# Kernel tuning notes

Hardware: AMD Instinct MI355X
Metric: run time of the kernel (lower is better)

The kernel has to match this reference:

```python
import jax, jax.numpy as jnp
import numpy as np

D = 512          # input_dim == hidden size of MinLSTM layers
OUT = 1          # output_dim of fc_out
B, T = 8, 4096
LN_EPS = 1e-5


def _linear_params(key, d_in, d_out):
    kw, kb = jax.random.split(key)
    lim = 1.0 / np.sqrt(d_in)
    W = jax.random.uniform(kw, (d_out, d_in), minval=-lim, maxval=lim, dtype=jnp.float32)
    b = jax.random.uniform(kb, (d_out,), minval=-lim, maxval=lim, dtype=jnp.float32)
    return W, b


def setup_inputs() -> dict:
    key = jax.random.key(0)
    ks = jax.random.split(key, 8)
    x = jax.random.normal(ks[0], (B, T, D), dtype=jnp.float32)
    Wf0, bf0 = _linear_params(ks[1], D, D)
    Wi0, bi0 = _linear_params(ks[2], D, D)
    Wh0, bh0 = _linear_params(ks[3], D, D)
    Wf1, bf1 = _linear_params(ks[4], D, D)
    Wi1, bi1 = _linear_params(ks[5], D, D)
    Wh1, bh1 = _linear_params(ks[6], D, D)
    W_out, b_out = _linear_params(ks[7], D, OUT)
    ln_g = jnp.ones((D,), dtype=jnp.float32)
    ln_b = jnp.zeros((D,), dtype=jnp.float32)
    return {
        'x': x,
        'Wf0': Wf0, 'bf0': bf0, 'Wi0': Wi0, 'bi0': bi0, 'Wh0': Wh0, 'bh0': bh0,
        'Wf1': Wf1, 'bf1': bf1, 'Wi1': Wi1, 'bi1': bi1, 'Wh1': Wh1, 'bh1': bh1,
        'ln_g': ln_g, 'ln_b': ln_b, 'W_out': W_out, 'b_out': b_out,
    }


def _minlstm(x, Wf, bf, Wi, bi, Wh, bh):
    # minLSTM (parallel form, h0 = 0):
    #   f = sigma(W_f x), i = sigma(W_i x), h~ = W_h x
    #   f' = f/(f+i), i' = i/(f+i)
    #   h_t = f'_t * h_{t-1} + i'_t * h~_t   (linear recurrence -> associative scan)
    f = jax.nn.sigmoid(jnp.einsum('btd,ed->bte', x, Wf) + bf)
    i = jax.nn.sigmoid(jnp.einsum('btd,ed->bte', x, Wi) + bi)
    h_tilde = jnp.einsum('btd,ed->bte', x, Wh) + bh
    denom = f + i
    a = f / denom                      # decay coefficient f'
    u = (i / denom) * h_tilde          # input contribution i' * h~

    def combine(c1, c2):
        a1, u1 = c1
        a2, u2 = c2
        return a1 * a2, a2 * u1 + u2

    _, h = jax.lax.associative_scan(combine, (a, u), axis=1)
    return h  # [B, T, D]


def reference(x, Wf0, bf0, Wi0, bi0, Wh0, bh0,
              Wf1, bf1, Wi1, bi1, Wh1, bh1,
              ln_g, ln_b, W_out, b_out):
    h = _minlstm(x, Wf0, bf0, Wi0, bi0, Wh0, bh0)
    h = _minlstm(h, Wf1, bf1, Wi1, bi1, Wh1, bh1)
    h = jnp.where(jnp.isnan(h), x, h)      # NaN fallback to input
    h = x + h                               # residual
    # LayerNorm over last dim
    mu = jnp.mean(h, axis=-1, keepdims=True)
    var = jnp.mean(jnp.square(h - mu), axis=-1, keepdims=True)
    hn = (h - mu) * jax.lax.rsqrt(var + LN_EPS) * ln_g + ln_b
    # output projection [B, T, OUT]
    return jnp.einsum('btd,od->bto', hn, W_out) + b_out
```

## Files before the change

### kernel.cpp

```cpp
#include <hip/hip_runtime.h>
#include <hip/hip_bf16.h>
#include <stdint.h>


#define MROWS 32768
#define DDIM  512
#define TLEN  4096
#define BSZ   8
#define NCHUNK 64
#define CLEN   64

typedef __attribute__((ext_vector_type(8))) __bf16 bf16x8;
typedef __attribute__((ext_vector_type(16))) float f32x16;

static __device__ __forceinline__ unsigned short f2bf(float f) {
    unsigned int u = __float_as_uint(f);
    u = (u + 0x7FFFu + ((u >> 16) & 1u)) >> 16;
    return (unsigned short)u;
}
static __device__ __forceinline__ void gload_lds16(const void* gptr, void* ldsp) {
    __builtin_amdgcn_global_load_lds(
        (const __attribute__((address_space(1))) uint32_t*)gptr,
        (__attribute__((address_space(3))) uint32_t*)ldsp,
        16, 0, 0);
}

#define WAITV(n) asm volatile("s_waitcnt vmcnt(" #n ")" ::: "memory")

__global__ __launch_bounds__(256) void cast_perm(
    const float* __restrict__ x,
    const float* __restrict__ w0, const float* __restrict__ w1,
    const float* __restrict__ w2, const float* __restrict__ w3,
    const float* __restrict__ w4, const float* __restrict__ w5,
    uint4* __restrict__ xp, uint4* __restrict__ wp)
{
    int S = blockIdx.x * 256 + threadIdx.x;
    const float* src;
    uint4* dst;
    if (S < 2097152) {
        int Gr = S >> 11, rem = S & 2047;
        int Tk = rem >> 8, c = (rem >> 5) & 7, r = rem & 31;
        src = x + ((size_t)(Gr * 32 + r) * 512 + Tk * 64 + c * 8);
        dst = xp + S;
    } else {
        int SW = S - 2097152;
        int g = SW >> 15, rem2 = SW & 32767;
        int Gn = rem2 >> 11, rem = rem2 & 2047;
        int Tk = rem >> 8, c = (rem >> 5) & 7, r = rem & 31;
        const float* w = (g == 0) ? w0 : (g == 1) ? w1 : (g == 2) ? w2
                       : (g == 3) ? w3 : (g == 4) ? w4 : w5;
        src = w + ((size_t)(Gn * 32 + r) * 512 + Tk * 64 + c * 8);
        dst = wp + SW;
    }
    float4 v0 = *(const float4*)src;
    float4 v1 = *(const float4*)(src + 4);
    uint4 o;
    o.x = (unsigned)f2bf(v0.x) | ((unsigned)f2bf(v0.y) << 16);
    o.y = (unsigned)f2bf(v0.z) | ((unsigned)f2bf(v0.w) << 16);
    o.z = (unsigned)f2bf(v1.x) | ((unsigned)f2bf(v1.y) << 16);
    o.w = (unsigned)f2bf(v1.z) | ((unsigned)f2bf(v1.w) << 16);
    *dst = o;
}

__global__ __launch_bounds__(256, 2) void gates_gemm(
    const unsigned short* __restrict__ X,
    const unsigned short* __restrict__ Wf,
    const unsigned short* __restrict__ Wi,
    const unsigned short* __restrict__ Wh,
    const float* __restrict__ bf_, const float* __restrict__ bi_,
    const float* __restrict__ bh_,
    unsigned int* __restrict__ au_out,
    float* __restrict__ Asum, float* __restrict__ Usum)
{
    __shared__ __align__(16) unsigned short lds[2 * 20480];

    const int tid  = threadIdx.x;
    const int lane = tid & 63;
    const int wave = tid >> 6;
    const int wm = wave >> 1;
    const int wn = wave & 1;
    const int ln31 = lane & 31;
    const int kh = lane >> 5;

    const int w = blockIdx.x;
    const int xcd = w & 7;
    const int s = w >> 3;
    const int by = xcd * 32 + (s >> 3);
    const int bx = s & 7;
    const int mblk = by * 128;
    const int nblk = bx * 64;

    const int grA = mblk >> 5;
    const int gnB = nblk >> 5;
    const unsigned short* gA0 = X  + ((size_t)(grA + 0) * 2048 + tid) * 8;
    const unsigned short* gA1 = X  + ((size_t)(grA + 1) * 2048 + tid) * 8;
    const unsigned short* gA2 = X  + ((size_t)(grA + 2) * 2048 + tid) * 8;
    const unsigned short* gA3 = X  + ((size_t)(grA + 3) * 2048 + tid) * 8;
    const unsigned short* gF0 = Wf + ((size_t)(gnB + 0) * 2048 + tid) * 8;
    const unsigned short* gF1 = Wf + ((size_t)(gnB + 1) * 2048 + tid) * 8;
    const unsigned short* gI0 = Wi + ((size_t)(gnB + 0) * 2048 + tid) * 8;
    const unsigned short* gI1 = Wi + ((size_t)(gnB + 1) * 2048 + tid) * 8;
    const unsigned short* gH0 = Wh + ((size_t)(gnB + 0) * 2048 + tid) * 8;
    const unsigned short* gH1 = Wh + ((size_t)(gnB + 1) * 2048 + tid) * 8;

    const int tid8 = tid * 8;
    const int lane16 = lane * 8;

    f32x16 accF[2], accI[2], accH[2];
#pragma unroll
    for (int mi = 0; mi < 2; ++mi) {
#pragma unroll
        for (int e = 0; e < 16; ++e) { accF[mi][e] = 0.f; accI[mi][e] = 0.f; accH[mi][e] = 0.f; }
    }

#define STAGE(bb) do { \
    gload_lds16(gA0, lds + (bb) + tid8);             \
    gload_lds16(gA1, lds + (bb) + 2048  + tid8);     \
    gload_lds16(gA2, lds + (bb) + 4096  + tid8);     \
    gload_lds16(gA3, lds + (bb) + 6144  + tid8);     \
    gload_lds16(gF0, lds + (bb) + 8192  + tid8);     \
    gload_lds16(gF1, lds + (bb) + 10240 + tid8);     \
    gload_lds16(gI0, lds + (bb) + 12288 + tid8);     \
    gload_lds16(gI1, lds + (bb) + 14336 + tid8);     \
    gload_lds16(gH0, lds + (bb) + 16384 + tid8);     \
    gload_lds16(gH1, lds + (bb) + 18432 + tid8);     \
    gA0 += 2048; gA1 += 2048; gA2 += 2048; gA3 += 2048; gF0 += 2048; \
    gF1 += 2048; gI0 += 2048; gI1 += 2048; gH0 += 2048; gH1 += 2048; } while (0)

    STAGE(0);

#pragma unroll
    for (int t = 0; t < 8; ++t) {
        if (t < 7) {
            STAGE(((t + 1) & 1) * 20480);
            WAITV(10);
        } else {
            WAITV(0);
        }
        __builtin_amdgcn_s_barrier();
        __builtin_amdgcn_sched_barrier(0);

        const unsigned short* cb = lds + (t & 1) * 20480;
#pragma unroll
        for (int ks = 0; ks < 4; ++ks) {
            bf16x8 af0 = *reinterpret_cast<const bf16x8*>(cb + (wm * 8 + ks) * 512 + lane16);
            bf16x8 bF  = *reinterpret_cast<const bf16x8*>(cb + 8192  + (wn * 4 + ks) * 512 + lane16);
            bf16x8 af1 = *reinterpret_cast<const bf16x8*>(cb + (wm * 8 + 4 + ks) * 512 + lane16);
            bf16x8 bI  = *reinterpret_cast<const bf16x8*>(cb + 12288 + (wn * 4 + ks) * 512 + lane16);
            bf16x8 bH  = *reinterpret_cast<const bf16x8*>(cb + 16384 + (wn * 4 + ks) * 512 + lane16);
            __builtin_amdgcn_s_setprio(1);
            accF[0] = __builtin_amdgcn_mfma_f32_32x32x16_bf16(af0, bF, accF[0], 0, 0, 0);
            accF[1] = __builtin_amdgcn_mfma_f32_32x32x16_bf16(af1, bF, accF[1], 0, 0, 0);
            accI[0] = __builtin_amdgcn_mfma_f32_32x32x16_bf16(af0, bI, accI[0], 0, 0, 0);
            accI[1] = __builtin_amdgcn_mfma_f32_32x32x16_bf16(af1, bI, accI[1], 0, 0, 0);
            accH[0] = __builtin_amdgcn_mfma_f32_32x32x16_bf16(af0, bH, accH[0], 0, 0, 0);
            accH[1] = __builtin_amdgcn_mfma_f32_32x32x16_bf16(af1, bH, accH[1], 0, 0, 0);
            __builtin_amdgcn_s_setprio(0);
        }
        __builtin_amdgcn_sched_barrier(0);
        __builtin_amdgcn_s_barrier();
        __builtin_amdgcn_sched_barrier(0);
    }
#undef STAGE

    const int n = nblk + wn * 32 + ln31;
    const float bfv = bf_[n], biv = bi_[n], bhv = bh_[n];
    const bool up = (lane & 32) != 0;
    float ca = 1.f, cu = 0.f;
#pragma unroll
    for (int mi = 0; mi < 2; ++mi) {
#pragma unroll
        for (int j = 0; j < 4; ++j) {
            float sa = 1.f, su = 0.f;
#pragma unroll
            for (int r = 0; r < 4; ++r) {
                const int reg = 4 * j + r;
                const int m = mblk + wm * 64 + mi * 32 + 8 * j + 4 * kh + r;
                float zf = accF[mi][reg] + bfv;
                float zi = accI[mi][reg] + biv;
                float zh = accH[mi][reg] + bhv;
                float ef = __expf(-zf);
                float ei = __expf(-zi);
                float inv = __frcp_rn(2.0f + ef + ei);
                float av = (1.0f + ei) * inv;
                float uv = (1.0f + ef) * inv * zh;
                au_out[(size_t)m * 512 + n] =
                    ((unsigned int)f2bf(uv) << 16) | (unsigned int)f2bf(av);
                su = av * su + uv; sa *= av;
            }
            float oa = __shfl_xor(sa, 32), ou = __shfl_xor(su, 32);
            float ta = sa * oa;
            float tu = up ? (sa * ou + su) : (oa * su + ou);
            cu = ta * cu + tu; ca = ca * ta;
        }
    }
    if (lane < 32) {
        size_t ci = (size_t)(by * 2 + wm) * 512 + n;
        Asum[ci] = ca;
        Usum[ci] = cu;
    }
}

__global__ void scan_pass2(const float4* __restrict__ Asum, const float4* __restrict__ Usum,
                           float4* __restrict__ Hinit) {
    int t = blockIdx.x * 256 + threadIdx.x;
    int d4 = t & 127;
    int b = t >> 7;
    float4 h = {0.f, 0.f, 0.f, 0.f};
    for (int c = 0; c < NCHUNK; ++c) {
        size_t idx = (size_t)(b * NCHUNK + c) * 128 + d4;
        Hinit[idx] = h;
        float4 A = Asum[idx]; float4 U = Usum[idx];
        h.x = A.x * h.x + U.x; h.y = A.y * h.y + U.y;
        h.z = A.z * h.z + U.z; h.w = A.w * h.w + U.w;
    }
}

__global__ void scan_pass3(const uint4* __restrict__ au,
                           const float4* __restrict__ Hinit,
                           uint4* __restrict__ hp) {
    int gid = blockIdx.x * 256 + threadIdx.x;
    int d8 = gid & 63;
    int c  = (gid >> 6) & 63;
    int b  = gid >> 12;
    const int base_m = b * TLEN + c * CLEN;
    size_t aubase = (size_t)base_m * 128 + d8 * 2;
    size_t s4 = (size_t)(b * NCHUNK + c) * 128 + d8 * 2;
    float4 h0 = Hinit[s4], h1 = Hinit[s4 + 1];
    float h[8] = {h0.x, h0.y, h0.z, h0.w, h1.x, h1.y, h1.z, h1.w};
    const int Tk = d8 >> 3, cc = d8 & 7;
    for (int l = 0; l < CLEN; ++l) {
        int m = base_m + l;
        uint4 a0 = au[aubase + (size_t)l * 128];
        uint4 a1 = au[aubase + (size_t)l * 128 + 1];
        unsigned vv[8] = {a0.x, a0.y, a0.z, a0.w, a1.x, a1.y, a1.z, a1.w};
        unsigned ob[8];
#pragma unroll
        for (int j = 0; j < 8; ++j) {
            float av = __uint_as_float(vv[j] << 16);
            float uv = __uint_as_float(vv[j] & 0xFFFF0000u);
            h[j] = av * h[j] + uv;
            ob[j] = f2bf(h[j]);
        }
        uint4 o;
        o.x = ob[0] | (ob[1] << 16);
        o.y = ob[2] | (ob[3] << 16);
        o.z = ob[4] | (ob[5] << 16);
        o.w = ob[6] | (ob[7] << 16);
        int S = (m >> 5) * 2048 + Tk * 256 + cc * 32 + (m & 31);
        hp[S] = o;
    }
}

__global__ __launch_bounds__(128) void scan3_final(
    const uint4* __restrict__ au, const float4* __restrict__ Hinit,
    const float4* __restrict__ x4,
    const float* __restrict__ g, const float* __restrict__ bvec,
    const float* __restrict__ Wout, const float* __restrict__ bout,
    float* __restrict__ out)
{
    const int blk = blockIdx.x;
    const int b = blk >> 6, c = blk & 63;
    const int d4 = threadIdx.x;
    const int lane = threadIdx.x & 63;
    const int wv = threadIdx.x >> 6;

    float4 h0 = Hinit[(size_t)blk * 128 + d4];
    float h[4] = {h0.x, h0.y, h0.z, h0.w};
    float4 g4 = reinterpret_cast<const float4*>(g)[d4];
    float4 b4 = reinterpret_cast<const float4*>(bvec)[d4];
    float4 w4 = reinterpret_cast<const float4*>(Wout)[d4];
    const float ga[4] = {g4.x, g4.y, g4.z, g4.w};
    const float ba[4] = {b4.x, b4.y, b4.z, b4.w};
    const float wa[4] = {w4.x, w4.y, w4.z, w4.w};
    const float bo = bout[0];

    __shared__ float redS[2], redQ[2], redP[2];
    size_t base = ((size_t)b * TLEN + c * CLEN) * 128 + d4;

    for (int l = 0; l < CLEN; ++l) {
        size_t idx = base + (size_t)l * 128;
        uint4 v = au[idx];
        float4 xr = x4[idx];
        const unsigned int vv[4] = {v.x, v.y, v.z, v.w};
        const float xa[4] = {xr.x, xr.y, xr.z, xr.w};
        float r[4];
        float sfl = 0.f, q = 0.f;
#pragma unroll
        for (int j = 0; j < 4; ++j) {
            float av = __uint_as_float(vv[j] << 16);
            float uv = __uint_as_float(vv[j] & 0xFFFF0000u);
            h[j] = av * h[j] + uv;
            float hv = h[j];
            if (hv != hv) hv = xa[j];
            float rr = xa[j] + hv;
            r[j] = rr;
            sfl += rr; q += rr * rr;
        }
#pragma unroll
        for (int m = 32; m >= 1; m >>= 1) {
            sfl += __shfl_xor(sfl, m);
            q += __shfl_xor(q, m);
        }
        if (lane == 0) { redS[wv] = sfl; redQ[wv] = q; }
        __syncthreads();
        float st = redS[0] + redS[1];
        float qt = redQ[0] + redQ[1];
        float mu = st * (1.0f / 512.0f);
        float var = qt * (1.0f / 512.0f) - mu * mu;
        float rstd = rsqrtf(var + 1e-5f);
        float p = 0.f;
#pragma unroll
        for (int j = 0; j < 4; ++j)
            p += ((r[j] - mu) * rstd * ga[j] + ba[j]) * wa[j];
#pragma unroll
        for (int m = 32; m >= 1; m >>= 1) p += __shfl_xor(p, m);
        if (lane == 0) redP[wv] = p;
        __syncthreads();
        if (threadIdx.x == 0)
            out[(size_t)b * TLEN + c * CLEN + l] = redP[0] + redP[1] + bo;
    }
}

extern "C" void kernel_launch(void* const* d_in, const int* in_sizes, int n_in,
                              void* d_out, int out_size, void* d_ws, size_t ws_size,
                              hipStream_t stream) {
    const float* x    = (const float*)d_in[0];
    const float* Wf0  = (const float*)d_in[1];  const float* bf0 = (const float*)d_in[2];
    const float* Wi0  = (const float*)d_in[3];  const float* bi0 = (const float*)d_in[4];
    const float* Wh0  = (const float*)d_in[5];  const float* bh0 = (const float*)d_in[6];
    const float* Wf1  = (const float*)d_in[7];  const float* bf1 = (const float*)d_in[8];
    const float* Wi1  = (const float*)d_in[9];  const float* bi1 = (const float*)d_in[10];
    const float* Wh1  = (const float*)d_in[11]; const float* bh1 = (const float*)d_in[12];
    const float* ln_g = (const float*)d_in[13]; const float* ln_b = (const float*)d_in[14];
    const float* W_out = (const float*)d_in[15]; const float* b_out = (const float*)d_in[16];

    char* ws = (char*)d_ws;
    unsigned short* Xp = (unsigned short*)ws;  ws += (size_t)MROWS * DDIM * 2;
    unsigned short* Wp = (unsigned short*)ws;  ws += (size_t)6 * DDIM * DDIM * 2;
    unsigned int* aubuf = (unsigned int*)ws;   ws += (size_t)MROWS * DDIM * 4;
    float* Asum = (float*)ws;  ws += (size_t)BSZ * NCHUNK * DDIM * 4;
    float* Usum = (float*)ws;  ws += (size_t)BSZ * NCHUNK * DDIM * 4;
    float* Hinit = (float*)ws; ws += (size_t)BSZ * NCHUNK * DDIM * 4;
    unsigned short* h0p = (unsigned short*)ws; ws += (size_t)MROWS * DDIM * 2;

    const size_t GSTRIDE = (size_t)DDIM * DDIM;

    cast_perm<<<8960, 256, 0, stream>>>(
        x, Wf0, Wi0, Wh0, Wf1, Wi1, Wh1, (uint4*)Xp, (uint4*)Wp);

    gates_gemm<<<2048, 256, 0, stream>>>(Xp, Wp, Wp + GSTRIDE, Wp + 2 * GSTRIDE,
                                         bf0, bi0, bh0, aubuf, Asum, Usum);
    scan_pass2<<<4, 256, 0, stream>>>((const float4*)Asum, (const float4*)Usum, (float4*)Hinit);
    scan_pass3<<<128, 256, 0, stream>>>((const uint4*)aubuf, (const float4*)Hinit, (uint4*)h0p);

    gates_gemm<<<2048, 256, 0, stream>>>(h0p, Wp + 3 * GSTRIDE, Wp + 4 * GSTRIDE, Wp + 5 * GSTRIDE,
                                         bf1, bi1, bh1, aubuf, Asum, Usum);
    scan_pass2<<<4, 256, 0, stream>>>((const float4*)Asum, (const float4*)Usum, (float4*)Hinit);
    scan3_final<<<512, 128, 0, stream>>>((const uint4*)aubuf, (const float4*)Hinit,
                                         (const float4*)x, ln_g, ln_b, W_out, b_out,
                                         (float*)d_out);
}
```

Measured before the change: 253.2 us.

## Coalesce cast via LDS, parallelize chunk scan, decouple final layernorm from scan

Three separate changes. The cast/permute kernel now stages a 32-row tile in LDS, so its global reads are coalesced and each block does more work. The cross-chunk scan pass now splits each column across 8 lanes and combines them with a shuffle-based prefix scan, which raises the block count from 4 to 32 and shortens the serial chain. The final kernel first writes the residual rows as bf16 into LDS, then runs LayerNorm and the projection per row within a single wave, removing two block barriers per timestep. The price is more LDS use and bf16 rounding of the residual before LayerNorm, which may affect accuracy.

```diff
diff --git a/kernel.cpp b/kernel.cpp
--- a/kernel.cpp
+++ b/kernel.cpp
@@ -12,6 +12,7 @@
 
 typedef __attribute__((ext_vector_type(8))) __bf16 bf16x8;
 typedef __attribute__((ext_vector_type(16))) float f32x16;
+typedef __attribute__((ext_vector_type(4))) unsigned short ushort4_t;
 
 static __device__ __forceinline__ unsigned short f2bf(float f) {
     unsigned int u = __float_as_uint(f);
@@ -34,32 +35,39 @@
     const float* __restrict__ w4, const float* __restrict__ w5,
     uint4* __restrict__ xp, uint4* __restrict__ wp)
 {
-    int S = blockIdx.x * 256 + threadIdx.x;
+    __shared__ unsigned short t[32 * 520];
+    const int blk = blockIdx.x;
+    const int tid = threadIdx.x;
     const float* src;
     uint4* dst;
-    if (S < 2097152) {
-        int Gr = S >> 11, rem = S & 2047;
-        int Tk = rem >> 8, c = (rem >> 5) & 7, r = rem & 31;
-        src = x + ((size_t)(Gr * 32 + r) * 512 + Tk * 64 + c * 8);
-        dst = xp + S;
+    if (blk < 1024) {
+        src = x + (size_t)blk * 32 * 512;
+        dst = xp + (size_t)blk * 2048;
     } else {
-        int SW = S - 2097152;
-        int g = SW >> 15, rem2 = SW & 32767;
-        int Gn = rem2 >> 11, rem = rem2 & 2047;
-        int Tk = rem >> 8, c = (rem >> 5) & 7, r = rem & 31;
+        int gb = blk - 1024;
+        int g = gb >> 4;
         const float* w = (g == 0) ? w0 : (g == 1) ? w1 : (g == 2) ? w2
                        : (g == 3) ? w3 : (g == 4) ? w4 : w5;
-        src = w + ((size_t)(Gn * 32 + r) * 512 + Tk * 64 + c * 8);
-        dst = wp + SW;
-    }
-    float4 v0 = *(const float4*)src;
-    float4 v1 = *(const float4*)(src + 4);
-    uint4 o;
-    o.x = (unsigned)f2bf(v0.x) | ((unsigned)f2bf(v0.y) << 16);
-    o.y = (unsigned)f2bf(v0.z) | ((unsigned)f2bf(v0.w) << 16);
-    o.z = (unsigned)f2bf(v1.x) | ((unsigned)f2bf(v1.y) << 16);
-    o.w = (unsigned)f2bf(v1.z) | ((unsigned)f2bf(v1.w) << 16);
-    *dst = o;
+        src = w + (size_t)(gb & 15) * 32 * 512;
+        dst = wp + (size_t)gb * 2048;
+    }
+#pragma unroll
+    for (int p = 0; p < 16; ++p) {
+        int idx = p * 256 + tid;
+        int r = idx >> 7, c4 = idx & 127;
+        float4 v = reinterpret_cast<const float4*>(src)[(size_t)r * 128 + c4];
+        ushort4_t o;
+        o.x = f2bf(v.x); o.y = f2bf(v.y); o.z = f2bf(v.z); o.w = f2bf(v.w);
+        *reinterpret_cast<ushort4_t*>(&t[r * 520 + c4 * 4]) = o;
+    }
+    __syncthreads();
+#pragma unroll
+    for (int q = 0; q < 8; ++q) {
+        int s = q * 256 + tid;
+        int Tk = s >> 8, c = (s >> 5) & 7, r = s & 31;
+        uint4 o = *reinterpret_cast<const uint4*>(&t[r * 520 + Tk * 64 + c * 8]);
+        dst[s] = o;
+    }
 }
 
 __global__ __launch_bounds__(256, 2) void gates_gemm(
@@ -201,18 +209,49 @@
     }
 }
 
-__global__ void scan_pass2(const float4* __restrict__ Asum, const float4* __restrict__ Usum,
-                           float4* __restrict__ Hinit) {
-    int t = blockIdx.x * 256 + threadIdx.x;
-    int d4 = t & 127;
-    int b = t >> 7;
-    float4 h = {0.f, 0.f, 0.f, 0.f};
-    for (int c = 0; c < NCHUNK; ++c) {
-        size_t idx = (size_t)(b * NCHUNK + c) * 128 + d4;
+__global__ __launch_bounds__(256) void scan_pass2(
+    const float4* __restrict__ Asum, const float4* __restrict__ Usum,
+    float4* __restrict__ Hinit)
+{
+    int gid = blockIdx.x * 256 + threadIdx.x;
+    int col = gid >> 3;
+    int t8  = gid & 7;
+    int b = col >> 7, d4 = col & 127;
+    int lane = threadIdx.x & 63;
+
+    float4 a[8], u[8];
+    float4 Ac = {1.f, 1.f, 1.f, 1.f}, Uc = {0.f, 0.f, 0.f, 0.f};
+#pragma unroll
+    for (int j = 0; j < 8; ++j) {
+        size_t idx = (size_t)(b * 64 + t8 * 8 + j) * 128 + d4;
+        a[j] = Asum[idx]; u[j] = Usum[idx];
+        Uc.x = a[j].x * Uc.x + u[j].x; Uc.y = a[j].y * Uc.y + u[j].y;
+        Uc.z = a[j].z * Uc.z + u[j].z; Uc.w = a[j].w * Uc.w + u[j].w;
+        Ac.x *= a[j].x; Ac.y *= a[j].y; Ac.z *= a[j].z; Ac.w *= a[j].w;
+    }
+#pragma unroll
+    for (int d = 1; d < 8; d <<= 1) {
+        float4 Ao, Uo;
+        Ao.x = __shfl(Ac.x, lane - d); Ao.y = __shfl(Ac.y, lane - d);
+        Ao.z = __shfl(Ac.z, lane - d); Ao.w = __shfl(Ac.w, lane - d);
+        Uo.x = __shfl(Uc.x, lane - d); Uo.y = __shfl(Uc.y, lane - d);
+        Uo.z = __shfl(Uc.z, lane - d); Uo.w = __shfl(Uc.w, lane - d);
+        if (t8 >= d) {
+            Uc.x = Ac.x * Uo.x + Uc.x; Uc.y = Ac.y * Uo.y + Uc.y;
+            Uc.z = Ac.z * Uo.z + Uc.z; Uc.w = Ac.w * Uo.w + Uc.w;
+            Ac.x *= Ao.x; Ac.y *= Ao.y; Ac.z *= Ao.z; Ac.w *= Ao.w;
+        }
+    }
+    float4 h;
+    h.x = __shfl(Uc.x, lane - 1); h.y = __shfl(Uc.y, lane - 1);
+    h.z = __shfl(Uc.z, lane - 1); h.w = __shfl(Uc.w, lane - 1);
+    if (t8 == 0) { h.x = 0.f; h.y = 0.f; h.z = 0.f; h.w = 0.f; }
+#pragma unroll
+    for (int j = 0; j < 8; ++j) {
+        size_t idx = (size_t)(b * 64 + t8 * 8 + j) * 128 + d4;
         Hinit[idx] = h;
-        float4 A = Asum[idx]; float4 U = Usum[idx];
-        h.x = A.x * h.x + U.x; h.y = A.y * h.y + U.y;
-        h.z = A.z * h.z + U.z; h.w = A.w * h.w + U.w;
+        h.x = a[j].x * h.x + u[j].x; h.y = a[j].y * h.y + u[j].y;
+        h.z = a[j].z * h.z + u[j].z; h.w = a[j].w * h.w + u[j].w;
     }
 }
 
@@ -259,33 +298,23 @@
     const float* __restrict__ Wout, const float* __restrict__ bout,
     float* __restrict__ out)
 {
+    __shared__ unsigned short rl[64 * 512];
     const int blk = blockIdx.x;
     const int b = blk >> 6, c = blk & 63;
     const int d4 = threadIdx.x;
-    const int lane = threadIdx.x & 63;
-    const int wv = threadIdx.x >> 6;
 
     float4 h0 = Hinit[(size_t)blk * 128 + d4];
     float h[4] = {h0.x, h0.y, h0.z, h0.w};
-    float4 g4 = reinterpret_cast<const float4*>(g)[d4];
-    float4 b4 = reinterpret_cast<const float4*>(bvec)[d4];
-    float4 w4 = reinterpret_cast<const float4*>(Wout)[d4];
-    const float ga[4] = {g4.x, g4.y, g4.z, g4.w};
-    const float ba[4] = {b4.x, b4.y, b4.z, b4.w};
-    const float wa[4] = {w4.x, w4.y, w4.z, w4.w};
-    const float bo = bout[0];
-
-    __shared__ float redS[2], redQ[2], redP[2];
     size_t base = ((size_t)b * TLEN + c * CLEN) * 128 + d4;
 
+#pragma unroll 4
     for (int l = 0; l < CLEN; ++l) {
         size_t idx = base + (size_t)l * 128;
         uint4 v = au[idx];
         float4 xr = x4[idx];
-        const unsigned int vv[4] = {v.x, v.y, v.z, v.w};
+        const unsigned vv[4] = {v.x, v.y, v.z, v.w};
         const float xa[4] = {xr.x, xr.y, xr.z, xr.w};
-        float r[4];
-        float sfl = 0.f, q = 0.f;
+        ushort4_t o;
 #pragma unroll
         for (int j = 0; j < 4; ++j) {
             float av = __uint_as_float(vv[j] << 16);
@@ -293,32 +322,54 @@
             h[j] = av * h[j] + uv;
             float hv = h[j];
             if (hv != hv) hv = xa[j];
-            float rr = xa[j] + hv;
-            r[j] = rr;
-            sfl += rr; q += rr * rr;
-        }
+            o[j] = f2bf(xa[j] + hv);
+        }
+        *reinterpret_cast<ushort4_t*>(&rl[l * 512 + d4 * 4]) = o;
+    }
+    __syncthreads();
+
+    const int lane = threadIdx.x & 63;
+    const int wv = threadIdx.x >> 6;
+    float4 g0 = reinterpret_cast<const float4*>(g)[lane * 2];
+    float4 g1 = reinterpret_cast<const float4*>(g)[lane * 2 + 1];
+    float4 b0 = reinterpret_cast<const float4*>(bvec)[lane * 2];
+    float4 b1 = reinterpret_cast<const float4*>(bvec)[lane * 2 + 1];
+    float4 w0 = reinterpret_cast<const float4*>(Wout)[lane * 2];
+    float4 w1 = reinterpret_cast<const float4*>(Wout)[lane * 2 + 1];
+    const float gg[8] = {g0.x, g0.y, g0.z, g0.w, g1.x, g1.y, g1.z, g1.w};
+    const float bb[8] = {b0.x, b0.y, b0.z, b0.w, b1.x, b1.y, b1.z, b1.w};
+    const float ww[8] = {w0.x, w0.y, w0.z, w0.w, w1.x, w1.y, w1.z, w1.w};
+    const float bo = bout[0];
+
+    for (int rr = 0; rr < 32; ++rr) {
+        const int row = wv * 32 + rr;
+        uint4 rv = *reinterpret_cast<const uint4*>(&rl[row * 512 + lane * 8]);
+        const unsigned rw[4] = {rv.x, rv.y, rv.z, rv.w};
+        float r[8];
+#pragma unroll
+        for (int j = 0; j < 4; ++j) {
+            r[2 * j]     = __uint_as_float(rw[j] << 16);
+            r[2 * j + 1] = __uint_as_float(rw[j] & 0xFFFF0000u);
+        }
+        float s = 0.f, q = 0.f;
+#pragma unroll
+        for (int j = 0; j < 8; ++j) { s += r[j]; q += r[j] * r[j]; }
 #pragma unroll
         for (int m = 32; m >= 1; m >>= 1) {
-            sfl += __shfl_xor(sfl, m);
+            s += __shfl_xor(s, m);
             q += __shfl_xor(q, m);
         }
-        if (lane == 0) { redS[wv] = sfl; redQ[wv] = q; }
-        __syncthreads();
-        float st = redS[0] + redS[1];
-        float qt = redQ[0] + redQ[1];
-        float mu = st * (1.0f / 512.0f);
-        float var = qt * (1.0f / 512.0f) - mu * mu;
+        float mu = s * (1.0f / 512.0f);
+        float var = q * (1.0f / 512.0f) - mu * mu;
         float rstd = rsqrtf(var + 1e-5f);
         float p = 0.f;
 #pragma unroll
-        for (int j = 0; j < 4; ++j)
-            p += ((r[j] - mu) * rstd * ga[j] + ba[j]) * wa[j];
+        for (int j = 0; j < 8; ++j)
+            p += ((r[j] - mu) * rstd * gg[j] + bb[j]) * ww[j];
 #pragma unroll
         for (int m = 32; m >= 1; m >>= 1) p += __shfl_xor(p, m);
-        if (lane == 0) redP[wv] = p;
-        __syncthreads();
-        if (threadIdx.x == 0)
-            out[(size_t)b * TLEN + c * CLEN + l] = redP[0] + redP[1] + bo;
+        if (lane == 0)
+            out[(size_t)b * TLEN + c * CLEN + row] = p + bo;
     }
 }
 
@@ -346,17 +397,17 @@
 
     const size_t GSTRIDE = (size_t)DDIM * DDIM;
 
-    cast_perm<<<8960, 256, 0, stream>>>(
+    cast_perm<<<1120, 256, 0, stream>>>(
         x, Wf0, Wi0, Wh0, Wf1, Wi1, Wh1, (uint4*)Xp, (uint4*)Wp);
 
     gates_gemm<<<2048, 256, 0, stream>>>(Xp, Wp, Wp + GSTRIDE, Wp + 2 * GSTRIDE,
                                          bf0, bi0, bh0, aubuf, Asum, Usum);
-    scan_pass2<<<4, 256, 0, stream>>>((const float4*)Asum, (const float4*)Usum, (float4*)Hinit);
+    scan_pass2<<<32, 256, 0, stream>>>((const float4*)Asum, (const float4*)Usum, (float4*)Hinit);
     scan_pass3<<<128, 256, 0, stream>>>((const uint4*)aubuf, (const float4*)Hinit, (uint4*)h0p);
 
     gates_gemm<<<2048, 256, 0, stream>>>(h0p, Wp + 3 * GSTRIDE, Wp + 4 * GSTRIDE, Wp + 5 * GSTRIDE,
                                          bf1, bi1, bh1, aubuf, Asum, Usum);
-    scan_pass2<<<4, 256, 0, stream>>>((const float4*)Asum, (const float4*)Usum, (float4*)Hinit);
+    scan_pass2<<<32, 256, 0, stream>>>((const float4*)Asum, (const float4*)Usum, (float4*)Hinit);
     scan3_final<<<512, 128, 0, stream>>>((const uint4*)aubuf, (const float4*)Hinit,
                                          (const float4*)x, ln_g, ln_b, W_out, b_out,
                                          (float*)d_out);
```

Result: faster. 216.7 us (-14.4%).
